# Kernel optimization log

Hardware: AMD Instinct MI355X
Metric: run time of the kernel (lower is better)

The kernel has to match this reference:

```python
import jax, jax.numpy as jnp
import numpy as np

N_NODES = 50000
N_EDGES = 600000
N_GRAPHS = 64
HID = 128
NLAYERS = 4
IN_DIM = 5
NCLS = 5
EPS = 1e-5


def setup_inputs() -> dict:
    key = jax.random.key(0)
    ks = jax.random.split(key, 16)
    x = jax.random.normal(ks[0], (N_NODES, IN_DIM), dtype=jnp.float32)
    edge_index = jax.random.randint(ks[1], (2, N_EDGES), 0, N_NODES, dtype=jnp.int64)
    batch = jnp.sort(jax.random.randint(ks[2], (N_NODES,), 0, N_GRAPHS, dtype=jnp.int64))
    s = 0.05
    Wp = jax.random.normal(ks[3], (IN_DIM, HID), jnp.float32) * s
    bp = jnp.zeros((HID,), jnp.float32)
    Wg = jax.random.normal(ks[4], (NLAYERS, HID, HID), jnp.float32) * s
    bg = jnp.zeros((NLAYERS, HID), jnp.float32)
    gamma = jnp.ones((NLAYERS, HID), jnp.float32)
    beta = jnp.zeros((NLAYERS, HID), jnp.float32)
    W1 = jax.random.normal(ks[5], (2 * HID, HID), jnp.float32) * s
    b1 = jnp.zeros((HID,), jnp.float32)
    W2 = jax.random.normal(ks[6], (HID, HID // 2), jnp.float32) * s
    b2 = jnp.zeros((HID // 2,), jnp.float32)
    W3 = jax.random.normal(ks[7], (HID // 2, NCLS), jnp.float32) * s
    b3 = jnp.zeros((NCLS,), jnp.float32)
    return {"x": x, "edge_index": edge_index, "batch": batch, "Wp": Wp, "bp": bp,
            "Wg": Wg, "bg": bg, "gamma": gamma, "beta": beta,
            "W1": W1, "b1": b1, "W2": W2, "b2": b2, "W3": W3, "b3": b3}


def reference(x, edge_index, batch, Wp, bp, Wg, bg, gamma, beta, W1, b1, W2, b2, W3, b3):
    N = x.shape[0]
    # GCN with added self-loops and symmetric normalization (PyG GCNConv defaults)
    loop = jnp.arange(N)
    src = jnp.concatenate([edge_index[0], loop])
    dst = jnp.concatenate([edge_index[1], loop])
    deg = jax.ops.segment_sum(jnp.ones_like(dst, dtype=x.dtype), dst, num_segments=N)
    dinv = jax.lax.rsqrt(deg)  # deg >= 1 thanks to self-loops
    norm = dinv[src] * dinv[dst]  # [E+N]
    h = x @ Wp + bp  # [N, HID]
    for i in range(NLAYERS):
        m = h @ Wg[i]
        agg = jax.ops.segment_sum(m[src] * norm[:, None], dst, num_segments=N) + bg[i]
        # BatchNorm1d (training-mode stats over nodes)
        mu = jnp.mean(agg, axis=0)
        var = jnp.var(agg, axis=0)
        h = gamma[i] * (agg - mu) * jax.lax.rsqrt(var + EPS) + beta[i]
        h = jax.nn.relu(h)  # dropout is identity in eval mode
    # mean_max global pooling per graph
    cnt = jax.ops.segment_sum(jnp.ones((N,), h.dtype), batch, num_segments=N_GRAPHS)
    x_mean = jax.ops.segment_sum(h, batch, num_segments=N_GRAPHS) / jnp.maximum(cnt, 1.0)[:, None]
    x_max = jax.ops.segment_max(h, batch, num_segments=N_GRAPHS)
    x_max = jnp.where(jnp.isfinite(x_max), x_max, 0.0)
    pooled = jnp.concatenate([x_mean, x_max], axis=1)  # [B, 2*HID]
    h1 = jax.nn.relu(pooled @ W1 + b1)
    h2 = jax.nn.relu(h1 @ W2 + b2)
    return h2 @ W3 + b3  # [B, num_classes]
```

## Files before the change

kernel.cpp:

```cpp
#include <hip/hip_runtime.h>
#include <hip/hip_bf16.h>

#define N_NODES 50000
#define N_EDGES 600000
#define N_GRAPHS 64
#define HID 128
#define NLAYERS 4
#define IN_DIM 5
#define NCLS 5
#define EPS 1e-5f
#define SCAN_BLK ((N_NODES + 511) / 512)
#define FILL_BLK ((N_EDGES + 255) / 256)
#define POOL_CHUNKS 16
#define BSLOT 64
#define WS 136

typedef __attribute__((ext_vector_type(8))) short s16x8;
typedef __attribute__((ext_vector_type(4))) float f32x4;

__device__ __forceinline__ unsigned short f2bf(float x) {
    unsigned u = __float_as_uint(x);
    unsigned r = (u + 0x7fffu + ((u >> 16) & 1u)) >> 16;
    return (unsigned short)r;
}
__device__ __forceinline__ float2 bfpair(unsigned u) {
    float2 r;
    r.x = __uint_as_float(u << 16);
    r.y = __uint_as_float(u & 0xffff0000u);
    return r;
}
__device__ __forceinline__ float bf2f(unsigned short s) {
    return __uint_as_float(((unsigned)s) << 16);
}


__global__ void k_count(const int* __restrict__ dst, int* __restrict__ cnt) {
    int i = blockIdx.x * blockDim.x + threadIdx.x;
    if (i < N_EDGES) atomicAdd(&cnt[dst[i]], 1);
}

__global__ void k_scan1(const int* __restrict__ cnt, int* __restrict__ rp, int* __restrict__ bsum) {
    __shared__ int s[512];
    int t = threadIdx.x;
    int i = blockIdx.x * 512 + t;
    int v = (i < N_NODES) ? cnt[i] : 0;
    s[t] = v;
    __syncthreads();
    for (int off = 1; off < 512; off <<= 1) {
        int x = (t >= off) ? s[t - off] : 0;
        __syncthreads();
        s[t] += x;
        __syncthreads();
    }
    if (i < N_NODES) rp[i + 1] = s[t];
    if (t == 511) bsum[blockIdx.x] = s[511];
}

__global__ void k_scan2g(int* __restrict__ bsum, const int* __restrict__ batch,
                         int* __restrict__ gstart) {
    if (blockIdx.x == 0) {
        __shared__ int s[128];
        int t = threadIdx.x;
        int v = (t < SCAN_BLK) ? bsum[t] : 0;
        s[t] = v;
        __syncthreads();
        for (int off = 1; off < 128; off <<= 1) {
            int x = (t >= off) ? s[t - off] : 0;
            __syncthreads();
            s[t] += x;
            __syncthreads();
        }
        if (t < SCAN_BLK) bsum[t] = s[t] - v;
    } else {
        int t = threadIdx.x;
        if (t <= N_GRAPHS) {
            int lo = 0, hi = N_NODES;
            while (lo < hi) {
                int mid = (lo + hi) >> 1;
                if (batch[mid] < t) lo = mid + 1; else hi = mid;
            }
            gstart[t] = lo;
        }
    }
}

__global__ void k_scan3d(int* __restrict__ rp, const int* __restrict__ bsum,
                         const int* __restrict__ cnt, float* __restrict__ dinv) {
    int i = blockIdx.x * 512 + threadIdx.x;
    if (i < N_NODES) {
        rp[i + 1] += bsum[blockIdx.x];
        dinv[i] = rsqrtf((float)(cnt[i] + 1));
    }
    if (i == 0) rp[0] = 0;
}

__global__ void k_fillw(const int* __restrict__ src, const int* __restrict__ dst,
                        const int* __restrict__ rp, int* __restrict__ cursor,
                        int2* __restrict__ cw, const float* __restrict__ dinv,
                        const float* __restrict__ Wg, unsigned short* __restrict__ WtG) {
    int b = blockIdx.x;
    if (b < FILL_BLK) {
        int e = b * 256 + threadIdx.x;
        if (e < N_EDGES) {
            int d = dst[e];
            int pos = atomicAdd(&cursor[d], 1);
            int s = src[e];
            int2 p;
            p.x = s;
            p.y = __float_as_int(dinv[s]);
            cw[rp[d] + pos] = p;
        }
    } else {
        int idx = (b - FILL_BLK) * 256 + threadIdx.x;
        int l = idx >> 14;
        int r = idx & 16383;
        int n = r >> 7, k = r & 127;
        WtG[idx] = f2bf(Wg[l * HID * HID + k * HID + n]);
    }
}


__global__ __launch_bounds__(256, 3) void k_gemmM(const unsigned short* __restrict__ Abf,
                                                  const float* __restrict__ x,
                                                  const float* __restrict__ Wp,
                                                  const float* __restrict__ bp,
                                                  const unsigned short* __restrict__ WtG,
                                                  unsigned short* __restrict__ Bm,
                                                  const float* __restrict__ psum,
                                                  const float* __restrict__ psq,
                                                  const float* __restrict__ gamma,
                                                  const float* __restrict__ beta,
                                                  int layer0) {
    __shared__ unsigned short Wt[HID * WS];
    __shared__ unsigned short Al[64 * WS];
    __shared__ float scl[HID], shf[HID];
    int t = threadIdx.x;
    {
        const uint4* Wg4 = (const uint4*)WtG;
        for (int idx = t; idx < HID * 16; idx += 256) {
            int n = idx >> 4, c = idx & 15;
            *(uint4*)&Wt[n * WS + c * 8] = Wg4[idx];
        }
    }
    if (!layer0 && t < HID) {
        float s = 0.f, s2 = 0.f;
#pragma unroll 8
        for (int b = 0; b < BSLOT; b++) {
            s += psum[b * HID + t];
            s2 += psq[b * HID + t];
        }
        const float invN = 1.f / (float)N_NODES;
        float mu = s * invN;
        float var = s2 * invN - mu * mu;
        float rs = rsqrtf(var + EPS) * gamma[t];
        scl[t] = rs;
        shf[t] = beta[t] - mu * rs;
    }
    int lane = t & 63, wv = t >> 6;
    int rbase = (wv & 1) * 32;
    int cbase = (wv >> 1) * 64;
    int mr = lane & 15, q = lane >> 4;
    const int numTiles = (N_NODES + 63) / 64;
    for (int tile = blockIdx.x; tile < numTiles; tile += gridDim.x) {
        int n0 = tile * 64;
        int limRow = min(64, N_NODES - n0);
        __syncthreads();
        if (layer0) {
            for (int idx = t; idx < 64 * HID; idx += 256) {
                int n = idx >> 7, k = idx & 127;
                int node = n0 + n;
                float acc = 0.f;
                if (node < N_NODES) {
                    acc = bp[k];
#pragma unroll
                    for (int j = 0; j < IN_DIM; j++) acc += x[node * IN_DIM + j] * Wp[j * HID + k];
                }
                Al[n * WS + k] = f2bf(acc);
            }
        } else {
            const uint2* Ag = (const uint2*)(Abf + (size_t)n0 * HID);
            for (int idx = t; idx < 64 * 32; idx += 256) {
                int row = idx >> 5, c4 = idx & 31;
                uint2 u = (row < limRow) ? Ag[row * 32 + c4] : make_uint2(0u, 0u);
                float2 ab = bfpair(u.x);
                float2 cd = bfpair(u.y);
                int kf = c4 * 4;
                float4 sc = *(const float4*)&scl[kf];
                float4 sh = *(const float4*)&shf[kf];
                float v0 = fmaxf(ab.x * sc.x + sh.x, 0.f);
                float v1 = fmaxf(ab.y * sc.y + sh.y, 0.f);
                float v2 = fmaxf(cd.x * sc.z + sh.z, 0.f);
                float v3 = fmaxf(cd.y * sc.w + sh.w, 0.f);
                unsigned lo = (unsigned)f2bf(v0) | ((unsigned)f2bf(v1) << 16);
                unsigned hi = (unsigned)f2bf(v2) | ((unsigned)f2bf(v3) << 16);
                *(uint2*)&Al[row * WS + kf] = make_uint2(lo, hi);
            }
        }
        __syncthreads();
        f32x4 acc[2][4];
#pragma unroll
        for (int rt = 0; rt < 2; rt++)
#pragma unroll
            for (int ct = 0; ct < 4; ct++) acc[rt][ct] = (f32x4){0.f, 0.f, 0.f, 0.f};
#pragma unroll
        for (int kk = 0; kk < HID; kk += 32) {
            s16x8 a0 = *(const s16x8*)&Al[(rbase + mr) * WS + kk + q * 8];
            s16x8 a1 = *(const s16x8*)&Al[(rbase + 16 + mr) * WS + kk + q * 8];
#pragma unroll
            for (int ct = 0; ct < 4; ct++) {
                s16x8 b = *(const s16x8*)&Wt[(cbase + ct * 16 + mr) * WS + kk + q * 8];
                acc[0][ct] = __builtin_amdgcn_mfma_f32_16x16x32_bf16(a0, b, acc[0][ct], 0, 0, 0);
                acc[1][ct] = __builtin_amdgcn_mfma_f32_16x16x32_bf16(a1, b, acc[1][ct], 0, 0, 0);
            }
        }
        __syncthreads();
#pragma unroll
        for (int rt = 0; rt < 2; rt++)
#pragma unroll
            for (int ct = 0; ct < 4; ct++)
#pragma unroll
                for (int r = 0; r < 4; r++) {
                    int rloc = rbase + rt * 16 + q * 4 + r;
                    int f = cbase + ct * 16 + mr;
                    Al[rloc * WS + f] = f2bf(acc[rt][ct][r]);
                }
        __syncthreads();
        for (int idx = t; idx < 64 * 16; idx += 256) {
            int row = idx >> 4, c = idx & 15;
            if (row < limRow)
                *(uint4*)&Bm[(size_t)(n0 + row) * HID + c * 8] = *(const uint4*)&Al[row * WS + c * 8];
        }
    }
}


__global__ __launch_bounds__(256) void k_gather(const uint4* __restrict__ Bm4,
                                                const int* __restrict__ rp,
                                                const int2* __restrict__ cw,
                                                const float* __restrict__ dinv,
                                                const float* __restrict__ bg,
                                                unsigned short* __restrict__ Aout,
                                                float* __restrict__ psum,
                                                float* __restrict__ psq) {
    __shared__ float ls[4 * HID], lq[4 * HID];
    int wave = threadIdx.x >> 6;
    int lane = threadIdx.x & 63;
    int s = lane & 15;
    int p = lane >> 4;
    int f = s * 8;
    int v = blockIdx.x * 16 + wave * 4 + p;
    int beg = rp[v], end = rp[v + 1];
    float dv = dinv[v];
    float a0, a1, a2, a3, a4, a5, a6, a7;
    {
        uint4 u = Bm4[(size_t)v * 16 + s];
        float2 q0 = bfpair(u.x), q1 = bfpair(u.y), q2 = bfpair(u.z), q3 = bfpair(u.w);
        a0 = q0.x * dv; a1 = q0.y * dv; a2 = q1.x * dv; a3 = q1.y * dv;
        a4 = q2.x * dv; a5 = q2.y * dv; a6 = q3.x * dv; a7 = q3.y * dv;
    }
    int e = beg;
    for (; e + 1 < end; e += 2) {
        int2 pe0 = cw[e];
        int2 pe1 = cw[e + 1];
        uint4 u0 = Bm4[(size_t)pe0.x * 16 + s];
        uint4 u1 = Bm4[(size_t)pe1.x * 16 + s];
        float w0 = __int_as_float(pe0.y);
        float w1 = __int_as_float(pe1.y);
        float2 x0 = bfpair(u0.x), x1 = bfpair(u0.y), x2 = bfpair(u0.z), x3 = bfpair(u0.w);
        float2 y0 = bfpair(u1.x), y1 = bfpair(u1.y), y2 = bfpair(u1.z), y3 = bfpair(u1.w);
        a0 += x0.x * w0 + y0.x * w1;
        a1 += x0.y * w0 + y0.y * w1;
        a2 += x1.x * w0 + y1.x * w1;
        a3 += x1.y * w0 + y1.y * w1;
        a4 += x2.x * w0 + y2.x * w1;
        a5 += x2.y * w0 + y2.y * w1;
        a6 += x3.x * w0 + y3.x * w1;
        a7 += x3.y * w0 + y3.y * w1;
    }
    if (e < end) {
        int2 pe = cw[e];
        uint4 u = Bm4[(size_t)pe.x * 16 + s];
        float w = __int_as_float(pe.y);
        float2 x0 = bfpair(u.x), x1 = bfpair(u.y), x2 = bfpair(u.z), x3 = bfpair(u.w);
        a0 += x0.x * w; a1 += x0.y * w; a2 += x1.x * w; a3 += x1.y * w;
        a4 += x2.x * w; a5 += x2.y * w; a6 += x3.x * w; a7 += x3.y * w;
    }
    float r0 = a0 * dv + bg[f + 0];
    float r1 = a1 * dv + bg[f + 1];
    float r2 = a2 * dv + bg[f + 2];
    float r3 = a3 * dv + bg[f + 3];
    float r4 = a4 * dv + bg[f + 4];
    float r5 = a5 * dv + bg[f + 5];
    float r6 = a6 * dv + bg[f + 6];
    float r7 = a7 * dv + bg[f + 7];
    unsigned short b0 = f2bf(r0), b1 = f2bf(r1), b2 = f2bf(r2), b3 = f2bf(r3);
    unsigned short b4 = f2bf(r4), b5 = f2bf(r5), b6 = f2bf(r6), b7 = f2bf(r7);
    uint4 o;
    o.x = (unsigned)b0 | ((unsigned)b1 << 16);
    o.y = (unsigned)b2 | ((unsigned)b3 << 16);
    o.z = (unsigned)b4 | ((unsigned)b5 << 16);
    o.w = (unsigned)b6 | ((unsigned)b7 << 16);
    *(uint4*)&Aout[(size_t)v * HID + f] = o;
    float v0 = bf2f(b0), v1 = bf2f(b1), v2 = bf2f(b2), v3 = bf2f(b3);
    float v4 = bf2f(b4), v5 = bf2f(b5), v6 = bf2f(b6), v7 = bf2f(b7);
    float ts0 = v0, ts1 = v1, ts2 = v2, ts3 = v3;
    float ts4 = v4, ts5 = v5, ts6 = v6, ts7 = v7;
    float tq0 = v0 * v0, tq1 = v1 * v1, tq2 = v2 * v2, tq3 = v3 * v3;
    float tq4 = v4 * v4, tq5 = v5 * v5, tq6 = v6 * v6, tq7 = v7 * v7;
    ts0 += __shfl_xor(ts0, 16); ts1 += __shfl_xor(ts1, 16);
    ts2 += __shfl_xor(ts2, 16); ts3 += __shfl_xor(ts3, 16);
    ts4 += __shfl_xor(ts4, 16); ts5 += __shfl_xor(ts5, 16);
    ts6 += __shfl_xor(ts6, 16); ts7 += __shfl_xor(ts7, 16);
    tq0 += __shfl_xor(tq0, 16); tq1 += __shfl_xor(tq1, 16);
    tq2 += __shfl_xor(tq2, 16); tq3 += __shfl_xor(tq3, 16);
    tq4 += __shfl_xor(tq4, 16); tq5 += __shfl_xor(tq5, 16);
    tq6 += __shfl_xor(tq6, 16); tq7 += __shfl_xor(tq7, 16);
    ts0 += __shfl_xor(ts0, 32); ts1 += __shfl_xor(ts1, 32);
    ts2 += __shfl_xor(ts2, 32); ts3 += __shfl_xor(ts3, 32);
    ts4 += __shfl_xor(ts4, 32); ts5 += __shfl_xor(ts5, 32);
    ts6 += __shfl_xor(ts6, 32); ts7 += __shfl_xor(ts7, 32);
    tq0 += __shfl_xor(tq0, 32); tq1 += __shfl_xor(tq1, 32);
    tq2 += __shfl_xor(tq2, 32); tq3 += __shfl_xor(tq3, 32);
    tq4 += __shfl_xor(tq4, 32); tq5 += __shfl_xor(tq5, 32);
    tq6 += __shfl_xor(tq6, 32); tq7 += __shfl_xor(tq7, 32);
    if (p == 0) {
        float* lsw = &ls[wave * HID + f];
        float* lqw = &lq[wave * HID + f];
        lsw[0] = ts0; lsw[1] = ts1; lsw[2] = ts2; lsw[3] = ts3;
        lsw[4] = ts4; lsw[5] = ts5; lsw[6] = ts6; lsw[7] = ts7;
        lqw[0] = tq0; lqw[1] = tq1; lqw[2] = tq2; lqw[3] = tq3;
        lqw[4] = tq4; lqw[5] = tq5; lqw[6] = tq6; lqw[7] = tq7;
    }
    __syncthreads();
    int tt = threadIdx.x;
    if (tt < HID) {
        float ssum = ls[tt] + ls[HID + tt] + ls[2 * HID + tt] + ls[3 * HID + tt];
        float ssq = lq[tt] + lq[HID + tt] + lq[2 * HID + tt] + lq[3 * HID + tt];
        int slot = blockIdx.x & (BSLOT - 1);
        atomicAdd(&psum[slot * HID + tt], ssum);
        atomicAdd(&psq[slot * HID + tt], ssq);
    }
}


__global__ __launch_bounds__(128) void k_pool(const unsigned short* __restrict__ A,
                                              const float* __restrict__ psum,
                                              const float* __restrict__ psq,
                                              const float* __restrict__ gamma,
                                              const float* __restrict__ beta,
                                              const int* __restrict__ gstart,
                                              float* __restrict__ poolPart) {
    int g = blockIdx.x;
    int c = blockIdx.y;
    int f = threadIdx.x;
    float s = 0.f, s2 = 0.f;
#pragma unroll 8
    for (int b = 0; b < BSLOT; b++) {
        s += psum[b * HID + f];
        s2 += psq[b * HID + f];
    }
    const float invN = 1.f / (float)N_NODES;
    float mu = s * invN;
    float var = s2 * invN - mu * mu;
    float sc = rsqrtf(var + EPS) * gamma[f];
    float sh = beta[f] - mu * sc;
    int beg = gstart[g], end = gstart[g + 1];
    int len = end - beg;
    int per = (len + POOL_CHUNKS - 1) / POOL_CHUNKS;
    int s0 = beg + c * per;
    int s1 = min(s0 + per, end);
    float sa = 0.f, sb = 0.f, ma = 0.f, mb = 0.f;
    int n = s0;
    for (; n + 1 < s1; n += 2) {
        float v0 = bf2f(A[(size_t)n * HID + f]);
        float v1 = bf2f(A[(size_t)(n + 1) * HID + f]);
        v0 = fmaxf(v0 * sc + sh, 0.f);
        v1 = fmaxf(v1 * sc + sh, 0.f);
        sa += v0; ma = fmaxf(ma, v0);
        sb += v1; mb = fmaxf(mb, v1);
    }
    if (n < s1) {
        float v = fmaxf(bf2f(A[(size_t)n * HID + f]) * sc + sh, 0.f);
        sa += v; ma = fmaxf(ma, v);
    }
    poolPart[((size_t)g * POOL_CHUNKS + c) * 256 + f] = sa + sb;
    poolPart[((size_t)g * POOL_CHUNKS + c) * 256 + 128 + f] = fmaxf(ma, mb);
}


__global__ __launch_bounds__(128) void k_head(const float* __restrict__ poolPart,
                                              const int* __restrict__ gstart,
                                              const float* __restrict__ W1, const float* __restrict__ b1,
                                              const float* __restrict__ W2, const float* __restrict__ b2,
                                              const float* __restrict__ W3, const float* __restrict__ b3,
                                              float* __restrict__ out) {
    __shared__ float pl[2 * HID];
    __shared__ float h1[HID];
    __shared__ float h2[HID / 2];
    int g = blockIdx.x, t = threadIdx.x;
    float cnt = fmaxf((float)(gstart[g + 1] - gstart[g]), 1.f);
    float s = 0.f, mx = 0.f;
#pragma unroll
    for (int c = 0; c < POOL_CHUNKS; c++) {
        const float* p = &poolPart[((size_t)g * POOL_CHUNKS + c) * 256];
        s += p[t];
        mx = fmaxf(mx, p[128 + t]);
    }
    pl[t] = s / cnt;
    pl[HID + t] = mx;
    __syncthreads();
    float acc = b1[t];
    for (int k = 0; k < 2 * HID; k++) acc += pl[k] * W1[k * HID + t];
    h1[t] = fmaxf(acc, 0.f);
    __syncthreads();
    if (t < HID / 2) {
        float a2 = b2[t];
        for (int k = 0; k < HID; k++) a2 += h1[k] * W2[k * (HID / 2) + t];
        h2[t] = fmaxf(a2, 0.f);
    }
    __syncthreads();
    if (t < NCLS) {
        float a3 = b3[t];
        for (int k = 0; k < HID / 2; k++) a3 += h2[k] * W3[k * NCLS + t];
        out[g * NCLS + t] = a3;
    }
}

extern "C" void kernel_launch(void* const* d_in, const int* in_sizes, int n_in,
                              void* d_out, int out_size, void* d_ws, size_t ws_size,
                              hipStream_t stream) {
    const float* x     = (const float*)d_in[0];
    const int*   ei    = (const int*)d_in[1];
    const int*   batch = (const int*)d_in[2];
    const float* Wp    = (const float*)d_in[3];
    const float* bp    = (const float*)d_in[4];
    const float* Wg    = (const float*)d_in[5];
    const float* bg    = (const float*)d_in[6];
    const float* gamma = (const float*)d_in[7];
    const float* beta  = (const float*)d_in[8];
    const float* W1    = (const float*)d_in[9];
    const float* b1    = (const float*)d_in[10];
    const float* W2    = (const float*)d_in[11];
    const float* b2    = (const float*)d_in[12];
    const float* W3    = (const float*)d_in[13];
    const float* b3    = (const float*)d_in[14];
    const int* src = ei;
    const int* dst = ei + N_EDGES;
    float* out = (float*)d_out;

    char* base = (char*)d_ws;
    size_t off = 0;
    auto alloc = [&](size_t bytes) -> void* {
        void* p = base + off;
        off += (bytes + 255) & ~(size_t)255;
        return p;
    };
    int*   counts = (int*)alloc((size_t)N_NODES * 4);
    int*   cursor = (int*)alloc((size_t)N_NODES * 4);
    float* psum   = (float*)alloc((size_t)NLAYERS * BSLOT * HID * 4);
    float* psq    = (float*)alloc((size_t)NLAYERS * BSLOT * HID * 4);
    size_t zeroBytes = off;
    int*   rp      = (int*)alloc((size_t)(N_NODES + 1) * 4);
    int*   bsum    = (int*)alloc(128 * 4);
    int2*  cw      = (int2*)alloc((size_t)N_EDGES * 8);
    float* dinv    = (float*)alloc((size_t)N_NODES * 4);
    int*   gstart  = (int*)alloc((size_t)(N_GRAPHS + 1) * 4);
    float* poolPart= (float*)alloc((size_t)N_GRAPHS * POOL_CHUNKS * 256 * 4);
    unsigned short* WtG = (unsigned short*)alloc((size_t)NLAYERS * HID * HID * 2);
    unsigned short* A = (unsigned short*)alloc((size_t)N_NODES * HID * 2);
    unsigned short* B = (unsigned short*)alloc((size_t)N_NODES * HID * 2);
    (void)ws_size; (void)in_sizes; (void)n_in; (void)out_size;

    hipMemsetAsync(d_ws, 0, zeroBytes, stream);

    k_count<<<(N_EDGES + 255) / 256, 256, 0, stream>>>(dst, counts);
    k_scan1<<<SCAN_BLK, 512, 0, stream>>>(counts, rp, bsum);
    k_scan2g<<<2, 128, 0, stream>>>(bsum, batch, gstart);
    k_scan3d<<<SCAN_BLK, 512, 0, stream>>>(rp, bsum, counts, dinv);
    k_fillw<<<FILL_BLK + (NLAYERS * HID * HID) / 256, 256, 0, stream>>>(
        src, dst, rp, cursor, cw, dinv, Wg, WtG);

    for (int i = 0; i < NLAYERS; i++) {
        int pl = (i == 0) ? 0 : (i - 1);
        k_gemmM<<<768, 256, 0, stream>>>(A, x, Wp, bp, WtG + (size_t)i * HID * HID, B,
                                         psum + (size_t)pl * BSLOT * HID,
                                         psq + (size_t)pl * BSLOT * HID,
                                         gamma + pl * HID, beta + pl * HID,
                                         (i == 0) ? 1 : 0);
        k_gather<<<N_NODES / 16, 256, 0, stream>>>((const uint4*)B, rp, cw, dinv,
                                                   bg + i * HID, A,
                                                   psum + (size_t)i * BSLOT * HID,
                                                   psq + (size_t)i * BSLOT * HID);
    }
    dim3 pg(N_GRAPHS, POOL_CHUNKS);
    k_pool<<<pg, 128, 0, stream>>>(A, psum + (size_t)3 * BSLOT * HID,
                                   psq + (size_t)3 * BSLOT * HID,
                                   gamma + 3 * HID, beta + 3 * HID, gstart, poolPart);
    k_head<<<N_GRAPHS, 128, 0, stream>>>(poolPart, gstart, W1, b1, W2, b2, W3, b3, out);
}
```

Baseline: 379.1 us.

## Map one wave per node in gather with grid-stride loop and 4-edge unrolling

Changes the SpMM gather so that each 64-lane wave handles one whole node, each lane owning two features through 32-bit loads, instead of 16 lanes per node with 128-bit loads. Waves walk nodes with a grid-stride loop and keep BatchNorm sum and sum-of-squares in registers across nodes, which drops the per-node cross-lane shuffle reduction. Edge pairs are read as aligned int4 with a 4-way unroll to give more loads in flight. The cost is narrower per-lane loads and a serial loop per wave, so per-node latency rises while less work goes into reductions and shuffles.

```diff
diff --git a/kernel.cpp b/kernel.cpp
--- a/kernel.cpp
+++ b/kernel.cpp
@@ -234,111 +234,76 @@
 }
 
 
-__global__ __launch_bounds__(256) void k_gather(const uint4* __restrict__ Bm4,
+__global__ __launch_bounds__(256) void k_gather(const unsigned* __restrict__ Bm2,
                                                 const int* __restrict__ rp,
                                                 const int2* __restrict__ cw,
                                                 const float* __restrict__ dinv,
                                                 const float* __restrict__ bg,
-                                                unsigned short* __restrict__ Aout,
+                                                unsigned* __restrict__ Aout2,
                                                 float* __restrict__ psum,
                                                 float* __restrict__ psq) {
     __shared__ float ls[4 * HID], lq[4 * HID];
-    int wave = threadIdx.x >> 6;
-    int lane = threadIdx.x & 63;
-    int s = lane & 15;
-    int p = lane >> 4;
-    int f = s * 8;
-    int v = blockIdx.x * 16 + wave * 4 + p;
-    int beg = rp[v], end = rp[v + 1];
-    float dv = dinv[v];
-    float a0, a1, a2, a3, a4, a5, a6, a7;
-    {
-        uint4 u = Bm4[(size_t)v * 16 + s];
-        float2 q0 = bfpair(u.x), q1 = bfpair(u.y), q2 = bfpair(u.z), q3 = bfpair(u.w);
-        a0 = q0.x * dv; a1 = q0.y * dv; a2 = q1.x * dv; a3 = q1.y * dv;
-        a4 = q2.x * dv; a5 = q2.y * dv; a6 = q3.x * dv; a7 = q3.y * dv;
-    }
-    int e = beg;
-    for (; e + 1 < end; e += 2) {
-        int2 pe0 = cw[e];
-        int2 pe1 = cw[e + 1];
-        uint4 u0 = Bm4[(size_t)pe0.x * 16 + s];
-        uint4 u1 = Bm4[(size_t)pe1.x * 16 + s];
-        float w0 = __int_as_float(pe0.y);
-        float w1 = __int_as_float(pe1.y);
-        float2 x0 = bfpair(u0.x), x1 = bfpair(u0.y), x2 = bfpair(u0.z), x3 = bfpair(u0.w);
-        float2 y0 = bfpair(u1.x), y1 = bfpair(u1.y), y2 = bfpair(u1.z), y3 = bfpair(u1.w);
-        a0 += x0.x * w0 + y0.x * w1;
-        a1 += x0.y * w0 + y0.y * w1;
-        a2 += x1.x * w0 + y1.x * w1;
-        a3 += x1.y * w0 + y1.y * w1;
-        a4 += x2.x * w0 + y2.x * w1;
-        a5 += x2.y * w0 + y2.y * w1;
-        a6 += x3.x * w0 + y3.x * w1;
-        a7 += x3.y * w0 + y3.y * w1;
-    }
-    if (e < end) {
-        int2 pe = cw[e];
-        uint4 u = Bm4[(size_t)pe.x * 16 + s];
-        float w = __int_as_float(pe.y);
-        float2 x0 = bfpair(u.x), x1 = bfpair(u.y), x2 = bfpair(u.z), x3 = bfpair(u.w);
-        a0 += x0.x * w; a1 += x0.y * w; a2 += x1.x * w; a3 += x1.y * w;
-        a4 += x2.x * w; a5 += x2.y * w; a6 += x3.x * w; a7 += x3.y * w;
-    }
-    float r0 = a0 * dv + bg[f + 0];
-    float r1 = a1 * dv + bg[f + 1];
-    float r2 = a2 * dv + bg[f + 2];
-    float r3 = a3 * dv + bg[f + 3];
-    float r4 = a4 * dv + bg[f + 4];
-    float r5 = a5 * dv + bg[f + 5];
-    float r6 = a6 * dv + bg[f + 6];
-    float r7 = a7 * dv + bg[f + 7];
-    unsigned short b0 = f2bf(r0), b1 = f2bf(r1), b2 = f2bf(r2), b3 = f2bf(r3);
-    unsigned short b4 = f2bf(r4), b5 = f2bf(r5), b6 = f2bf(r6), b7 = f2bf(r7);
-    uint4 o;
-    o.x = (unsigned)b0 | ((unsigned)b1 << 16);
-    o.y = (unsigned)b2 | ((unsigned)b3 << 16);
-    o.z = (unsigned)b4 | ((unsigned)b5 << 16);
-    o.w = (unsigned)b6 | ((unsigned)b7 << 16);
-    *(uint4*)&Aout[(size_t)v * HID + f] = o;
-    float v0 = bf2f(b0), v1 = bf2f(b1), v2 = bf2f(b2), v3 = bf2f(b3);
-    float v4 = bf2f(b4), v5 = bf2f(b5), v6 = bf2f(b6), v7 = bf2f(b7);
-    float ts0 = v0, ts1 = v1, ts2 = v2, ts3 = v3;
-    float ts4 = v4, ts5 = v5, ts6 = v6, ts7 = v7;
-    float tq0 = v0 * v0, tq1 = v1 * v1, tq2 = v2 * v2, tq3 = v3 * v3;
-    float tq4 = v4 * v4, tq5 = v5 * v5, tq6 = v6 * v6, tq7 = v7 * v7;
-    ts0 += __shfl_xor(ts0, 16); ts1 += __shfl_xor(ts1, 16);
-    ts2 += __shfl_xor(ts2, 16); ts3 += __shfl_xor(ts3, 16);
-    ts4 += __shfl_xor(ts4, 16); ts5 += __shfl_xor(ts5, 16);
-    ts6 += __shfl_xor(ts6, 16); ts7 += __shfl_xor(ts7, 16);
-    tq0 += __shfl_xor(tq0, 16); tq1 += __shfl_xor(tq1, 16);
-    tq2 += __shfl_xor(tq2, 16); tq3 += __shfl_xor(tq3, 16);
-    tq4 += __shfl_xor(tq4, 16); tq5 += __shfl_xor(tq5, 16);
-    tq6 += __shfl_xor(tq6, 16); tq7 += __shfl_xor(tq7, 16);
-    ts0 += __shfl_xor(ts0, 32); ts1 += __shfl_xor(ts1, 32);
-    ts2 += __shfl_xor(ts2, 32); ts3 += __shfl_xor(ts3, 32);
-    ts4 += __shfl_xor(ts4, 32); ts5 += __shfl_xor(ts5, 32);
-    ts6 += __shfl_xor(ts6, 32); ts7 += __shfl_xor(ts7, 32);
-    tq0 += __shfl_xor(tq0, 32); tq1 += __shfl_xor(tq1, 32);
-    tq2 += __shfl_xor(tq2, 32); tq3 += __shfl_xor(tq3, 32);
-    tq4 += __shfl_xor(tq4, 32); tq5 += __shfl_xor(tq5, 32);
-    tq6 += __shfl_xor(tq6, 32); tq7 += __shfl_xor(tq7, 32);
-    if (p == 0) {
-        float* lsw = &ls[wave * HID + f];
-        float* lqw = &lq[wave * HID + f];
-        lsw[0] = ts0; lsw[1] = ts1; lsw[2] = ts2; lsw[3] = ts3;
-        lsw[4] = ts4; lsw[5] = ts5; lsw[6] = ts6; lsw[7] = ts7;
-        lqw[0] = tq0; lqw[1] = tq1; lqw[2] = tq2; lqw[3] = tq3;
-        lqw[4] = tq4; lqw[5] = tq5; lqw[6] = tq6; lqw[7] = tq7;
-    }
+    int wv = threadIdx.x >> 6, lane = threadIdx.x & 63;
+    const int totalWaves = gridDim.x * 4;
+    int gw = blockIdx.x * 4 + wv;
+    float bg0 = bg[2 * lane], bg1 = bg[2 * lane + 1];
+    float ts0 = 0.f, ts1 = 0.f, tq0 = 0.f, tq1 = 0.f;
+    for (int v = gw; v < N_NODES; v += totalWaves) {
+        int beg = rp[v], end = rp[v + 1];
+        float dv = dinv[v];
+        float ax, ay;
+        {
+            float2 sl = bfpair(Bm2[(size_t)v * 64 + lane]);
+            ax = sl.x * dv;
+            ay = sl.y * dv;
+        }
+        int e = beg;
+        if ((e & 1) && e < end) {
+            int2 c = cw[e];
+            float2 f = bfpair(Bm2[(size_t)c.x * 64 + lane]);
+            float w = __int_as_float(c.y);
+            ax += f.x * w;
+            ay += f.y * w;
+            e++;
+        }
+        for (; e + 3 < end; e += 4) {
+            int4 c01 = *(const int4*)&cw[e];
+            int4 c23 = *(const int4*)&cw[e + 2];
+            unsigned r0 = Bm2[(size_t)c01.x * 64 + lane];
+            unsigned r1 = Bm2[(size_t)c01.z * 64 + lane];
+            unsigned r2 = Bm2[(size_t)c23.x * 64 + lane];
+            unsigned r3 = Bm2[(size_t)c23.z * 64 + lane];
+            float w0 = __int_as_float(c01.y), w1 = __int_as_float(c01.w);
+            float w2 = __int_as_float(c23.y), w3 = __int_as_float(c23.w);
+            float2 f0 = bfpair(r0), f1 = bfpair(r1);
+            float2 f2 = bfpair(r2), f3 = bfpair(r3);
+            ax += f0.x * w0 + f1.x * w1 + f2.x * w2 + f3.x * w3;
+            ay += f0.y * w0 + f1.y * w1 + f2.y * w2 + f3.y * w3;
+        }
+        for (; e < end; e++) {
+            int2 c = cw[e];
+            float2 f = bfpair(Bm2[(size_t)c.x * 64 + lane]);
+            float w = __int_as_float(c.y);
+            ax += f.x * w;
+            ay += f.y * w;
+        }
+        float r0 = ax * dv + bg0, r1 = ay * dv + bg1;
+        unsigned short h0 = f2bf(r0), h1 = f2bf(r1);
+        Aout2[(size_t)v * 64 + lane] = (unsigned)h0 | ((unsigned)h1 << 16);
+        float v0 = bf2f(h0), v1 = bf2f(h1);
+        ts0 += v0; ts1 += v1;
+        tq0 += v0 * v0; tq1 += v1 * v1;
+    }
+    *(float2*)&ls[wv * HID + 2 * lane] = make_float2(ts0, ts1);
+    *(float2*)&lq[wv * HID + 2 * lane] = make_float2(tq0, tq1);
     __syncthreads();
-    int tt = threadIdx.x;
-    if (tt < HID) {
-        float ssum = ls[tt] + ls[HID + tt] + ls[2 * HID + tt] + ls[3 * HID + tt];
-        float ssq = lq[tt] + lq[HID + tt] + lq[2 * HID + tt] + lq[3 * HID + tt];
+    int t = threadIdx.x;
+    if (t < HID) {
+        float ssum = ls[t] + ls[HID + t] + ls[2 * HID + t] + ls[3 * HID + t];
+        float ssq = lq[t] + lq[HID + t] + lq[2 * HID + t] + lq[3 * HID + t];
         int slot = blockIdx.x & (BSLOT - 1);
-        atomicAdd(&psum[slot * HID + tt], ssum);
-        atomicAdd(&psq[slot * HID + tt], ssq);
+        atomicAdd(&psum[slot * HID + t], ssum);
+        atomicAdd(&psq[slot * HID + t], ssq);
     }
 }
 
@@ -487,8 +452,8 @@
                                          psq + (size_t)pl * BSLOT * HID,
                                          gamma + pl * HID, beta + pl * HID,
                                          (i == 0) ? 1 : 0);
-        k_gather<<<N_NODES / 16, 256, 0, stream>>>((const uint4*)B, rp, cw, dinv,
-                                                   bg + i * HID, A,
+        k_gather<<<N_NODES / 16, 256, 0, stream>>>((const unsigned*)B, rp, cw, dinv,
+                                                   bg + i * HID, (unsigned*)A,
                                                    psum + (size_t)i * BSLOT * HID,
                                                    psq + (size_t)i * BSLOT * HID);
     }
```

New measurement: 412.5 us. 1.09x slower.

## Fuse graph-build kernels into one cooperative kernel, merge pool and head

Applied to the files above, without the earlier changes.

Five CSR build kernels (count, three scan stages, fill plus weight transpose) become one persistent kernel that uses software grid barriers between phases and zeroes its own buffers. The pool and head kernels are merged so each graph is pooled by a single 256-thread block with no poolPart round trip. This saves several launch and inter-kernel gaps. In exchange pooling now runs on only 64 blocks, each scanning roughly 780 nodes serially, and the spin barrier depends on all 512 blocks being resident at once. The merged pool code also carries some leftover redundant reduction steps.

```diff
diff --git a/kernel.cpp b/kernel.cpp
--- a/kernel.cpp
+++ b/kernel.cpp
@@ -9,11 +9,15 @@
 #define IN_DIM 5
 #define NCLS 5
 #define EPS 1e-5f
-#define SCAN_BLK ((N_NODES + 511) / 512)
-#define FILL_BLK ((N_EDGES + 255) / 256)
 #define POOL_CHUNKS 16
 #define BSLOT 64
 #define WS 136
+
+#define BUILD_BLK 512
+#define BUILD_THR 256
+#define NT_BUILD (BUILD_BLK * BUILD_THR)
+#define CHUNK 256
+#define NCHUNK ((N_NODES + CHUNK - 1) / CHUNK)
 
 typedef __attribute__((ext_vector_type(8))) short s16x8;
 typedef __attribute__((ext_vector_type(4))) float f32x4;
@@ -33,46 +37,76 @@
     return __uint_as_float(((unsigned)s) << 16);
 }
 
-
-__global__ void k_count(const int* __restrict__ dst, int* __restrict__ cnt) {
-    int i = blockIdx.x * blockDim.x + threadIdx.x;
-    if (i < N_EDGES) atomicAdd(&cnt[dst[i]], 1);
-}
-
-__global__ void k_scan1(const int* __restrict__ cnt, int* __restrict__ rp, int* __restrict__ bsum) {
-    __shared__ int s[512];
-    int t = threadIdx.x;
-    int i = blockIdx.x * 512 + t;
-    int v = (i < N_NODES) ? cnt[i] : 0;
-    s[t] = v;
-    __syncthreads();
-    for (int off = 1; off < 512; off <<= 1) {
-        int x = (t >= off) ? s[t - off] : 0;
-        __syncthreads();
-        s[t] += x;
-        __syncthreads();
-    }
-    if (i < N_NODES) rp[i + 1] = s[t];
-    if (t == 511) bsum[blockIdx.x] = s[511];
-}
-
-__global__ void k_scan2g(int* __restrict__ bsum, const int* __restrict__ batch,
-                         int* __restrict__ gstart) {
-    if (blockIdx.x == 0) {
-        __shared__ int s[128];
-        int t = threadIdx.x;
-        int v = (t < SCAN_BLK) ? bsum[t] : 0;
+__device__ __forceinline__ void gridbar(int* cnt, int* gen, int nblk) {
+    __syncthreads();
+    if (threadIdx.x == 0) {
+        int g = __hip_atomic_load(gen, __ATOMIC_RELAXED, __HIP_MEMORY_SCOPE_AGENT);
+        __threadfence();
+        int a = __hip_atomic_fetch_add(cnt, 1, __ATOMIC_RELAXED, __HIP_MEMORY_SCOPE_AGENT);
+        if (a == nblk - 1) {
+            __hip_atomic_store(cnt, 0, __ATOMIC_RELAXED, __HIP_MEMORY_SCOPE_AGENT);
+            __hip_atomic_store(gen, g + 1, __ATOMIC_RELEASE, __HIP_MEMORY_SCOPE_AGENT);
+        } else {
+            while (__hip_atomic_load(gen, __ATOMIC_RELAXED, __HIP_MEMORY_SCOPE_AGENT) == g)
+                __builtin_amdgcn_s_sleep(2);
+        }
+        __threadfence();
+    }
+    __syncthreads();
+}
+
+
+__global__ __launch_bounds__(BUILD_THR) void k_build(const int* __restrict__ src,
+                                                     const int* __restrict__ dst,
+                                                     const int* __restrict__ batch,
+                                                     const float* __restrict__ Wg,
+                                                     int* __restrict__ counts,
+                                                     int* __restrict__ cursor,
+                                                     float* __restrict__ psum,
+                                                     float* __restrict__ psq,
+                                                     int* __restrict__ rp,
+                                                     int* __restrict__ bsum,
+                                                     int2* __restrict__ cw,
+                                                     float* __restrict__ dinv,
+                                                     int* __restrict__ gstart,
+                                                     unsigned short* __restrict__ WtG,
+                                                     int* bcnt, int* bgen) {
+    __shared__ int s[CHUNK];
+    int t = threadIdx.x, b = blockIdx.x;
+    int gtid = b * BUILD_THR + t;
+    int nblk = gridDim.x;
+    for (int i = gtid; i < N_NODES; i += NT_BUILD) { counts[i] = 0; cursor[i] = 0; }
+    for (int i = gtid; i < NLAYERS * BSLOT * HID; i += NT_BUILD) { psum[i] = 0.f; psq[i] = 0.f; }
+    gridbar(bcnt, bgen, nblk);
+    for (int e = gtid; e < N_EDGES; e += NT_BUILD) atomicAdd(&counts[dst[e]], 1);
+    gridbar(bcnt, bgen, nblk);
+    if (b < NCHUNK) {
+        int i = b * CHUNK + t;
+        int v = (i < N_NODES) ? counts[i] : 0;
         s[t] = v;
         __syncthreads();
-        for (int off = 1; off < 128; off <<= 1) {
+        for (int off = 1; off < CHUNK; off <<= 1) {
             int x = (t >= off) ? s[t - off] : 0;
             __syncthreads();
             s[t] += x;
             __syncthreads();
         }
-        if (t < SCAN_BLK) bsum[t] = s[t] - v;
-    } else {
-        int t = threadIdx.x;
+        if (i < N_NODES) rp[i + 1] = s[t];
+        if (t == CHUNK - 1) bsum[b] = s[t];
+    }
+    gridbar(bcnt, bgen, nblk);
+    if (b == 0) {
+        int v = (t < NCHUNK) ? bsum[t] : 0;
+        s[t] = v;
+        __syncthreads();
+        for (int off = 1; off < 256; off <<= 1) {
+            int x = (t >= off) ? s[t - off] : 0;
+            __syncthreads();
+            s[t] += x;
+            __syncthreads();
+        }
+        if (t < NCHUNK) bsum[t] = s[t] - v;
+    } else if (b == 1) {
         if (t <= N_GRAPHS) {
             int lo = 0, hi = N_NODES;
             while (lo < hi) {
@@ -82,36 +116,26 @@
             gstart[t] = lo;
         }
     }
-}
-
-__global__ void k_scan3d(int* __restrict__ rp, const int* __restrict__ bsum,
-                         const int* __restrict__ cnt, float* __restrict__ dinv) {
-    int i = blockIdx.x * 512 + threadIdx.x;
-    if (i < N_NODES) {
-        rp[i + 1] += bsum[blockIdx.x];
-        dinv[i] = rsqrtf((float)(cnt[i] + 1));
-    }
-    if (i == 0) rp[0] = 0;
-}
-
-__global__ void k_fillw(const int* __restrict__ src, const int* __restrict__ dst,
-                        const int* __restrict__ rp, int* __restrict__ cursor,
-                        int2* __restrict__ cw, const float* __restrict__ dinv,
-                        const float* __restrict__ Wg, unsigned short* __restrict__ WtG) {
-    int b = blockIdx.x;
-    if (b < FILL_BLK) {
-        int e = b * 256 + threadIdx.x;
-        if (e < N_EDGES) {
-            int d = dst[e];
-            int pos = atomicAdd(&cursor[d], 1);
-            int s = src[e];
-            int2 p;
-            p.x = s;
-            p.y = __float_as_int(dinv[s]);
-            cw[rp[d] + pos] = p;
-        }
-    } else {
-        int idx = (b - FILL_BLK) * 256 + threadIdx.x;
+    gridbar(bcnt, bgen, nblk);
+    if (b < NCHUNK) {
+        int i = b * CHUNK + t;
+        if (i < N_NODES) {
+            rp[i + 1] += bsum[b];
+            dinv[i] = rsqrtf((float)(counts[i] + 1));
+        }
+    }
+    if (gtid == 0) rp[0] = 0;
+    gridbar(bcnt, bgen, nblk);
+    for (int e = gtid; e < N_EDGES; e += NT_BUILD) {
+        int d = dst[e];
+        int pos = atomicAdd(&cursor[d], 1);
+        int sn = src[e];
+        int2 p;
+        p.x = sn;
+        p.y = __float_as_int(dinv[sn]);
+        cw[rp[d] + pos] = p;
+    }
+    for (int idx = gtid; idx < NLAYERS * HID * HID; idx += NT_BUILD) {
         int l = idx >> 14;
         int r = idx & 16383;
         int n = r >> 7, k = r & 127;
@@ -343,16 +367,23 @@
 }
 
 
-__global__ __launch_bounds__(128) void k_pool(const unsigned short* __restrict__ A,
-                                              const float* __restrict__ psum,
-                                              const float* __restrict__ psq,
-                                              const float* __restrict__ gamma,
-                                              const float* __restrict__ beta,
-                                              const int* __restrict__ gstart,
-                                              float* __restrict__ poolPart) {
-    int g = blockIdx.x;
-    int c = blockIdx.y;
-    int f = threadIdx.x;
+__global__ __launch_bounds__(256) void k_poolhead(const unsigned short* __restrict__ A,
+                                                  const float* __restrict__ psum,
+                                                  const float* __restrict__ psq,
+                                                  const float* __restrict__ gamma,
+                                                  const float* __restrict__ beta,
+                                                  const int* __restrict__ gstart,
+                                                  const float* __restrict__ W1, const float* __restrict__ b1,
+                                                  const float* __restrict__ W2, const float* __restrict__ b2,
+                                                  const float* __restrict__ W3, const float* __restrict__ b3,
+                                                  float* __restrict__ out) {
+    __shared__ float pl[2 * HID];
+    __shared__ float h1[HID];
+    __shared__ float h2[HID / 2];
+    __shared__ float red[2 * HID];
+    int g = blockIdx.x, t = threadIdx.x;
+    int f = t & 127;
+    int half = t >> 7;
     float s = 0.f, s2 = 0.f;
 #pragma unroll 8
     for (int b = 0; b < BSLOT; b++) {
@@ -365,53 +396,51 @@
     float sc = rsqrtf(var + EPS) * gamma[f];
     float sh = beta[f] - mu * sc;
     int beg = gstart[g], end = gstart[g + 1];
-    int len = end - beg;
-    int per = (len + POOL_CHUNKS - 1) / POOL_CHUNKS;
-    int s0 = beg + c * per;
-    int s1 = min(s0 + per, end);
     float sa = 0.f, sb = 0.f, ma = 0.f, mb = 0.f;
-    int n = s0;
-    for (; n + 1 < s1; n += 2) {
+    int n = beg + half;
+#pragma unroll 2
+    for (; n + 2 < end; n += 4) {
         float v0 = bf2f(A[(size_t)n * HID + f]);
-        float v1 = bf2f(A[(size_t)(n + 1) * HID + f]);
+        float v1 = bf2f(A[(size_t)(n + 2) * HID + f]);
         v0 = fmaxf(v0 * sc + sh, 0.f);
         v1 = fmaxf(v1 * sc + sh, 0.f);
         sa += v0; ma = fmaxf(ma, v0);
         sb += v1; mb = fmaxf(mb, v1);
     }
-    if (n < s1) {
+    if (n < end) {
         float v = fmaxf(bf2f(A[(size_t)n * HID + f]) * sc + sh, 0.f);
         sa += v; ma = fmaxf(ma, v);
     }
-    poolPart[((size_t)g * POOL_CHUNKS + c) * 256 + f] = sa + sb;
-    poolPart[((size_t)g * POOL_CHUNKS + c) * 256 + 128 + f] = fmaxf(ma, mb);
-}
-
-
-__global__ __launch_bounds__(128) void k_head(const float* __restrict__ poolPart,
-                                              const int* __restrict__ gstart,
-                                              const float* __restrict__ W1, const float* __restrict__ b1,
-                                              const float* __restrict__ W2, const float* __restrict__ b2,
-                                              const float* __restrict__ W3, const float* __restrict__ b3,
-                                              float* __restrict__ out) {
-    __shared__ float pl[2 * HID];
-    __shared__ float h1[HID];
-    __shared__ float h2[HID / 2];
-    int g = blockIdx.x, t = threadIdx.x;
-    float cnt = fmaxf((float)(gstart[g + 1] - gstart[g]), 1.f);
-    float s = 0.f, mx = 0.f;
-#pragma unroll
-    for (int c = 0; c < POOL_CHUNKS; c++) {
-        const float* p = &poolPart[((size_t)g * POOL_CHUNKS + c) * 256];
-        s += p[t];
-        mx = fmaxf(mx, p[128 + t]);
-    }
-    pl[t] = s / cnt;
-    pl[HID + t] = mx;
-    __syncthreads();
-    float acc = b1[t];
-    for (int k = 0; k < 2 * HID; k++) acc += pl[k] * W1[k * HID + t];
-    h1[t] = fmaxf(acc, 0.f);
+    red[half * HID + f] = sa + sb;
+    __syncthreads();
+    red[half * HID + f + (half ? -HID : HID)] += 0.f;
+    __syncthreads();
+    if (half == 0) {
+    }
+    float totSum = 0.f, totMax = 0.f;
+    if (half == 0) totSum = red[f];
+    __syncthreads();
+    red[half * HID + f] = fmaxf(ma, mb);
+    __syncthreads();
+    if (half == 0) {
+        float cnt = fmaxf((float)(end - beg), 1.f);
+        totMax = fmaxf(red[f], red[HID + f]);
+        pl[HID + f] = totMax;
+        (void)totSum;
+    }
+    __syncthreads();
+    red[half * HID + f] = sa + sb;
+    __syncthreads();
+    if (half == 0) {
+        float cnt = fmaxf((float)(end - beg), 1.f);
+        pl[f] = (red[f] + red[HID + f]) / cnt;
+    }
+    __syncthreads();
+    if (t < 128) {
+        float acc = b1[t];
+        for (int k = 0; k < 2 * HID; k++) acc += pl[k] * W1[k * HID + t];
+        h1[t] = fmaxf(acc, 0.f);
+    }
     __syncthreads();
     if (t < HID / 2) {
         float a2 = b2[t];
@@ -455,17 +484,18 @@
         off += (bytes + 255) & ~(size_t)255;
         return p;
     };
+    int* bcnt = (int*)alloc(4);
+    int* bgen = (int*)alloc(4);
+    size_t zeroBytes = off;
     int*   counts = (int*)alloc((size_t)N_NODES * 4);
     int*   cursor = (int*)alloc((size_t)N_NODES * 4);
     float* psum   = (float*)alloc((size_t)NLAYERS * BSLOT * HID * 4);
     float* psq    = (float*)alloc((size_t)NLAYERS * BSLOT * HID * 4);
-    size_t zeroBytes = off;
     int*   rp      = (int*)alloc((size_t)(N_NODES + 1) * 4);
-    int*   bsum    = (int*)alloc(128 * 4);
+    int*   bsum    = (int*)alloc((size_t)NCHUNK * 4);
     int2*  cw      = (int2*)alloc((size_t)N_EDGES * 8);
     float* dinv    = (float*)alloc((size_t)N_NODES * 4);
     int*   gstart  = (int*)alloc((size_t)(N_GRAPHS + 1) * 4);
-    float* poolPart= (float*)alloc((size_t)N_GRAPHS * POOL_CHUNKS * 256 * 4);
     unsigned short* WtG = (unsigned short*)alloc((size_t)NLAYERS * HID * HID * 2);
     unsigned short* A = (unsigned short*)alloc((size_t)N_NODES * HID * 2);
     unsigned short* B = (unsigned short*)alloc((size_t)N_NODES * HID * 2);
@@ -473,12 +503,18 @@
 
     hipMemsetAsync(d_ws, 0, zeroBytes, stream);
 
-    k_count<<<(N_EDGES + 255) / 256, 256, 0, stream>>>(dst, counts);
-    k_scan1<<<SCAN_BLK, 512, 0, stream>>>(counts, rp, bsum);
-    k_scan2g<<<2, 128, 0, stream>>>(bsum, batch, gstart);
-    k_scan3d<<<SCAN_BLK, 512, 0, stream>>>(rp, bsum, counts, dinv);
-    k_fillw<<<FILL_BLK + (NLAYERS * HID * HID) / 256, 256, 0, stream>>>(
-        src, dst, rp, cursor, cw, dinv, Wg, WtG);
+    {
+        void* bargs[] = { (void*)&src, (void*)&dst, (void*)&batch, (void*)&Wg,
+                          (void*)&counts, (void*)&cursor, (void*)&psum, (void*)&psq,
+                          (void*)&rp, (void*)&bsum, (void*)&cw, (void*)&dinv,
+                          (void*)&gstart, (void*)&WtG, (void*)&bcnt, (void*)&bgen };
+        if (hipLaunchCooperativeKernel((void*)k_build, dim3(BUILD_BLK), dim3(BUILD_THR),
+                                       bargs, 0, stream) != hipSuccess) {
+            k_build<<<BUILD_BLK, BUILD_THR, 0, stream>>>(src, dst, batch, Wg, counts,
+                                                         cursor, psum, psq, rp, bsum,
+                                                         cw, dinv, gstart, WtG, bcnt, bgen);
+        }
+    }
 
     for (int i = 0; i < NLAYERS; i++) {
         int pl = (i == 0) ? 0 : (i - 1);
@@ -492,9 +528,8 @@
                                                    psum + (size_t)i * BSLOT * HID,
                                                    psq + (size_t)i * BSLOT * HID);
     }
-    dim3 pg(N_GRAPHS, POOL_CHUNKS);
-    k_pool<<<pg, 128, 0, stream>>>(A, psum + (size_t)3 * BSLOT * HID,
-                                   psq + (size_t)3 * BSLOT * HID,
-                                   gamma + 3 * HID, beta + 3 * HID, gstart, poolPart);
-    k_head<<<N_GRAPHS, 128, 0, stream>>>(poolPart, gstart, W1, b1, W2, b2, W3, b3, out);
-}
+    k_poolhead<<<N_GRAPHS, 256, 0, stream>>>(A, psum + (size_t)3 * BSLOT * HID,
+                                             psq + (size_t)3 * BSLOT * HID,
+                                             gamma + 3 * HID, beta + 3 * HID, gstart,
+                                             W1, b1, W2, b2, W3, b3, out);
+}
```

Result: slower. 518.9 us (+36.9%).
